# Kernel tuning notes

Hardware: AMD Instinct MI355X
Metric: run time of the kernel (lower is better)

The kernel has to match this reference:

```python
import jax, jax.numpy as jnp
from jax import lax
import numpy as np

VOCAB = 100000
EMB = 256
HID = 512          # bidirectional total
H = HID // 2       # per-direction hidden
TAGS = 12
START_IDX = 10
STOP_IDX = 11
B, S = 32, 256
NEG = -10000.0


def setup_inputs() -> dict:
    key = jax.random.key(0)
    ks = jax.random.split(key, 14)
    sc = 0.1
    sentences = jax.random.randint(ks[0], (B, S), 0, VOCAB)
    emb = jax.random.normal(ks[1], (VOCAB, EMB), jnp.float32) * sc
    wih_f = jax.random.normal(ks[2], (4 * H, EMB), jnp.float32) * sc
    whh_f = jax.random.normal(ks[3], (4 * H, H), jnp.float32) * sc
    bih_f = jax.random.normal(ks[4], (4 * H,), jnp.float32) * sc
    bhh_f = jax.random.normal(ks[5], (4 * H,), jnp.float32) * sc
    wih_b = jax.random.normal(ks[6], (4 * H, EMB), jnp.float32) * sc
    whh_b = jax.random.normal(ks[7], (4 * H, H), jnp.float32) * sc
    bih_b = jax.random.normal(ks[8], (4 * H,), jnp.float32) * sc
    bhh_b = jax.random.normal(ks[9], (4 * H,), jnp.float32) * sc
    w_out = jax.random.normal(ks[10], (TAGS, HID), jnp.float32) * sc
    b_out = jax.random.normal(ks[11], (TAGS,), jnp.float32) * sc
    transitions = jax.random.normal(ks[12], (TAGS, TAGS), jnp.float32)
    transitions = transitions.at[START_IDX, :].set(NEG)   # never transition into START
    transitions = transitions.at[:, STOP_IDX].set(NEG)    # never transition out of STOP
    return dict(sentences=sentences, emb=emb, wih_f=wih_f, whh_f=whh_f,
                bih_f=bih_f, bhh_f=bhh_f, wih_b=wih_b, whh_b=whh_b,
                bih_b=bih_b, bhh_b=bhh_b, w_out=w_out, b_out=b_out,
                transitions=transitions)


def _lstm_dir(x, wih, whh, bih, bhh, reverse):
    # x: [B,S,E]; PyTorch gate order i,f,g,o
    xg = jnp.einsum('bse,ge->bsg', x, wih) + bih + bhh  # [B,S,4H]
    h0 = jnp.zeros((x.shape[0], whh.shape[1]), x.dtype)
    c0 = jnp.zeros_like(h0)

    def step(carry, g_t):
        h, c = carry
        g = g_t + h @ whh.T
        i, f, gg, o = jnp.split(g, 4, axis=-1)
        c = jax.nn.sigmoid(f) * c + jax.nn.sigmoid(i) * jnp.tanh(gg)
        h = jax.nn.sigmoid(o) * jnp.tanh(c)
        return (h, c), h

    _, hs = lax.scan(step, (h0, c0), jnp.swapaxes(xg, 0, 1), reverse=reverse)
    return jnp.swapaxes(hs, 0, 1)  # [B,S,H]


def _features(sentences, emb, wih_f, whh_f, bih_f, bhh_f,
              wih_b, whh_b, bih_b, bhh_b, w_out, b_out):
    x = emb[sentences]                                   # [B,S,E]
    hf = _lstm_dir(x, wih_f, whh_f, bih_f, bhh_f, False)
    hb = _lstm_dir(x, wih_b, whh_b, bih_b, bhh_b, True)
    h = jnp.concatenate([hf, hb], axis=-1)               # [B,S,HID]
    return jnp.einsum('bsh,th->bst', h, w_out) + b_out   # [B,S,TAGS]


def _viterbi(feats, transitions):
    # feats: [B,S,T]; returns (score [B], path [B,S] int32)
    T = feats.shape[-1]
    init = jnp.full((T,), NEG, feats.dtype).at[START_IDX].set(0.0)

    def step(fv, emit):
        scores = fv[None, :] + transitions               # [next_tag, prev_tag]
        bp = jnp.argmax(scores, axis=1).astype(jnp.int32)
        fv_new = jnp.max(scores, axis=1) + emit
        return fv_new, bp

    def per_seq(feat_seq):                               # [S,T]
        fv, bps = lax.scan(step, init, feat_seq)         # bps: [S,T]
        term = fv + transitions[STOP_IDX]
        best = jnp.argmax(term).astype(jnp.int32)
        score = term[best]

        def back(tag, bp_t):
            return bp_t[tag], tag

        _, path = lax.scan(back, best, bps, reverse=True)
        return score, path

    return jax.vmap(per_seq)(feats)


def reference(sentences, emb, wih_f, whh_f, bih_f, bhh_f,
              wih_b, whh_b, bih_b, bhh_b, w_out, b_out, transitions):
    feats = _features(sentences, emb, wih_f, whh_f, bih_f, bhh_f,
                      wih_b, whh_b, bih_b, bhh_b, w_out, b_out)
    score, path = _viterbi(feats, transitions)
    return score, path
```

## Files before the change

### kernel.cpp

```cpp
#include <hip/hip_runtime.h>
#include <math.h>

#define BATCH 32
#define SEQ 256
#define EMBD 256
#define HDIM 256
#define G4H 1024
#define TAGS 12
#define START_IDX 10
#define STOP_IDX 11
#define NEGV -10000.0f

#define KRES 16
#define KLDS_G 18
#define KSTR_G 10

#define WS_XG    0
#define WS_X     16777216
#define WS_WPACK 18874368
#define WS_HALL  19234816
#define WS_FEATS 23429120

__device__ __forceinline__ float bcast(float v, int l) {
    return __int_as_float(__builtin_amdgcn_readlane(__float_as_int(v), l));
}

__global__ void gather_x(const int* __restrict__ sent, const float* __restrict__ emb,
                         float* __restrict__ x) {
    int m = blockIdx.x;
    int lane = threadIdx.x;
    long long row = sent[m];
    float4 v = *(const float4*)(emb + row * EMBD + lane * 4);
    *(float4*)(x + (size_t)m * EMBD + lane * 4) = v;
}

__global__ void pack_whh(const float* __restrict__ whh_f, const float* __restrict__ whh_b,
                         float4* __restrict__ pack) {
    int idx = blockIdx.x * 256 + threadIdx.x;
    if (idx >= 2 * 4 * KSTR_G * 512) return;
    int g = idx & 511;
    int r2 = idx >> 9;
    int j = r2 % KSTR_G; r2 /= KSTR_G;
    int q = r2 & 3, dir = r2 >> 2;
    int R = ((g >> 6) & 3) * 256 + q * 64 + (g & 63);
    int k = (g >> 8) * 128 + KRES + 4 * KLDS_G + 4 * j;
    const float* w = dir ? whh_b : whh_f;
    pack[idx] = *(const float4*)(w + (size_t)R * HDIM + k);
}

__launch_bounds__(256)
__global__ void gemm_xg(const float* __restrict__ x,
                        const float* __restrict__ wih_f, const float* __restrict__ wih_b,
                        const float* __restrict__ bih_f, const float* __restrict__ bhh_f,
                        const float* __restrict__ bih_b, const float* __restrict__ bhh_b,
                        float* __restrict__ xg) {
    __shared__ __align__(16) float as[8][128];
    __shared__ __align__(16) float bs[8][128];
    int m0 = blockIdx.x * 128;
    int n0 = blockIdx.y * 128;
    int tid = threadIdx.x;
    int tx = tid & 15, ty = tid >> 4;
    int lr = tid >> 1;
    int lh = (tid & 1) * 4;

    const float* arow = x + (size_t)(m0 + lr) * EMBD;
    const float* brow;
    {
        int n = n0 + lr;
        const float* w = (n < G4H) ? wih_f : wih_b;
        brow = w + (size_t)(n & 1023) * EMBD;
    }

    float acc[8][8];
    #pragma unroll
    for (int i = 0; i < 8; i++)
        #pragma unroll
        for (int j = 0; j < 8; j++) acc[i][j] = 0.f;

    for (int k0 = 0; k0 < EMBD; k0 += 8) {
        float4 av = *(const float4*)(arow + k0 + lh);
        float4 bv = *(const float4*)(brow + k0 + lh);
        __syncthreads();
        as[lh + 0][lr] = av.x; as[lh + 1][lr] = av.y; as[lh + 2][lr] = av.z; as[lh + 3][lr] = av.w;
        bs[lh + 0][lr] = bv.x; bs[lh + 1][lr] = bv.y; bs[lh + 2][lr] = bv.z; bs[lh + 3][lr] = bv.w;
        __syncthreads();
        #pragma unroll
        for (int kk = 0; kk < 8; kk++) {
            float4 a0 = *(const float4*)&as[kk][ty * 8];
            float4 a1 = *(const float4*)&as[kk][ty * 8 + 4];
            float4 b0 = *(const float4*)&bs[kk][tx * 8];
            float4 b1 = *(const float4*)&bs[kk][tx * 8 + 4];
            float a[8] = {a0.x, a0.y, a0.z, a0.w, a1.x, a1.y, a1.z, a1.w};
            float b[8] = {b0.x, b0.y, b0.z, b0.w, b1.x, b1.y, b1.z, b1.w};
            #pragma unroll
            for (int i = 0; i < 8; i++)
                #pragma unroll
                for (int j = 0; j < 8; j++) acc[i][j] += a[i] * b[j];
        }
    }

    int n = n0 + tx * 8;
    int dir = n >> 10, g0 = n & 1023;
    const float* bih = dir ? bih_b : bih_f;
    const float* bhh = dir ? bhh_b : bhh_f;
    float bi[8], bh[8];
    #pragma unroll
    for (int j = 0; j < 8; j++) { bi[j] = bih[g0 + j]; bh[j] = bhh[g0 + j]; }
    float* ob = xg + (size_t)dir * 8192 * G4H;
    #pragma unroll
    for (int i = 0; i < 8; i++) {
        int m = m0 + ty * 8 + i;
        float v[8];
        #pragma unroll
        for (int j = 0; j < 8; j++) v[j] = (acc[i][j] + bi[j]) + bh[j];
        *(float4*)(ob + (size_t)m * G4H + g0)     = make_float4(v[0], v[1], v[2], v[3]);
        *(float4*)(ob + (size_t)m * G4H + g0 + 4) = make_float4(v[4], v[5], v[6], v[7]);
    }
}

__global__ void zero_sync(float* __restrict__ hx, int* __restrict__ flags) {
    int i = blockIdx.x * 256 + threadIdx.x;
    if (i < 64 * 512) hx[i] = 0.f;
    if (i < 64 * 4) flags[i] = 0;
}

#define DOT4(W, KL)                                              \
    a0 += (W).x * bcast(hv[((KL) + 0) >> 6], ((KL) + 0) & 63);   \
    a1 += (W).y * bcast(hv[((KL) + 1) >> 6], ((KL) + 1) & 63);   \
    a2 += (W).z * bcast(hv[((KL) + 2) >> 6], ((KL) + 2) & 63);   \
    a3 += (W).w * bcast(hv[((KL) + 3) >> 6], ((KL) + 3) & 63);

__launch_bounds__(512)
__global__ void lstm_rec(const float* __restrict__ xg,
                         const float* __restrict__ whh_f, const float* __restrict__ whh_b,
                         const float4* __restrict__ wpack,
                         float* __restrict__ h_all,
                         float* __restrict__ hx, int* __restrict__ flags) {
    int blk = blockIdx.x;
    int chain = blk & 63;
    int q = blk >> 6;
    int dir = chain & 1, b = chain >> 1;
    int g = threadIdx.x;
    int lane = g & 63;
    int r = g & 255;
    int kh = g >> 8;
    int G = r >> 6, ul = r & 63;
    int R = G * 256 + q * 64 + ul;

    const float* whh = dir ? whh_b : whh_f;
    const float* wrow = whh + (size_t)R * HDIM + kh * 128;
    const float4* wp = wpack + (size_t)(dir * 4 + q) * KSTR_G * 512 + g;
    const float* xgb = xg + (size_t)dir * 8192 * G4H + (size_t)b * SEQ * G4H + R;
    float* hxc = hx + chain * 512;
    int* fl = flags + chain * 4;

    __shared__ __align__(16) float4 wlds[KLDS_G * 512];
    __shared__ float part[512];

    #pragma unroll
    for (int j = 0; j < KLDS_G; j++)
        wlds[j * 512 + g] = *(const float4*)(wrow + KRES + j * 4);
    float4 wr[KRES / 4];
    #pragma unroll
    for (int i = 0; i < KRES / 4; i++)
        wr[i] = *(const float4*)(wrow + i * 4);

    float c = 0.f;
    __syncthreads();

    for (int t = 0; t < SEQ; t++) {
        int s = dir ? (SEQ - 1 - t) : t;

        float xval = 0.f;
        if (g < 256) xval = xgb[(size_t)s * G4H];
        float4 sb[4];
        #pragma unroll
        for (int p = 0; p < 4; p++) sb[p] = wp[(size_t)p * 512];

        if (t > 0) {
            if (g < 3) {
                int pq = g + (g >= q ? 1 : 0);
                while (__hip_atomic_load(fl + pq, __ATOMIC_ACQUIRE,
                                         __HIP_MEMORY_SCOPE_AGENT) < t) {}
            }
            __syncthreads();
        }

        int rp = (t + 1) & 1;
        float hv[2];
        #pragma unroll
        for (int j = 0; j < 2; j++)
            hv[j] = __hip_atomic_load(hxc + rp * 256 + kh * 128 + j * 64 + lane,
                                      __ATOMIC_RELAXED, __HIP_MEMORY_SCOPE_AGENT);

        float a0 = 0.f, a1 = 0.f, a2 = 0.f, a3 = 0.f;

        #pragma unroll
        for (int i = 0; i < KRES / 4; i++) {
            float4 w = wr[i];
            DOT4(w, i * 4)
        }
        #pragma unroll
        for (int j = 0; j < KLDS_G; j++) {
            float4 w = wlds[j * 512 + g];
            DOT4(w, KRES + j * 4)
        }
        #pragma unroll
        for (int j = 0; j < KSTR_G; j++) {
            float4 w = sb[j & 3];
            if (j + 4 < KSTR_G) sb[j & 3] = wp[(size_t)(j + 4) * 512];
            DOT4(w, KRES + 4 * KLDS_G + j * 4)
        }

        part[g] = (a0 + a1) + (a2 + a3);
        __syncthreads();
        if (g < 256) part[g] = part[g] + part[g + 256] + xval;
        __syncthreads();
        if (g < 64) {
            float gi = part[g], gf = part[64 + g], gg = part[128 + g], go = part[192 + g];
            float si = 1.f / (1.f + expf(-gi));
            float sf = 1.f / (1.f + expf(-gf));
            float so = 1.f / (1.f + expf(-go));
            c = sf * c + si * tanhf(gg);
            float h = so * tanhf(c);
            int u = q * 64 + g;
            h_all[((size_t)b * SEQ + s) * 512 + dir * HDIM + u] = h;
            __hip_atomic_store(hxc + (t & 1) * 256 + u, h,
                               __ATOMIC_RELAXED, __HIP_MEMORY_SCOPE_AGENT);
        }
        __syncthreads();
        if (g == 0)
            __hip_atomic_store(fl + q, t + 1,
                               __ATOMIC_RELEASE, __HIP_MEMORY_SCOPE_AGENT);
    }
}

__global__ void feats_kernel(const float* __restrict__ h_all, const float* __restrict__ w_out,
                             const float* __restrict__ b_out, float* __restrict__ feats) {
    int p = blockIdx.x;
    int lane = threadIdx.x;
    const float* h = h_all + (size_t)p * 512;
    for (int f = 0; f < TAGS; f++) {
        float s = 0.f;
        const float* w = w_out + f * 512;
        #pragma unroll
        for (int k = 0; k < 512; k += 64) s += h[k + lane] * w[k + lane];
        #pragma unroll
        for (int off = 32; off; off >>= 1) s += __shfl_down(s, off);
        if (lane == 0) feats[(size_t)p * TAGS + f] = s + b_out[f];
    }
}

__global__ void viterbi_kernel(const float* __restrict__ feats, const float* __restrict__ trans,
                               float* __restrict__ out) {
    int b = blockIdx.x;
    int t = threadIdx.x;
    __shared__ float fv[TAGS], fvn[TAGS], tr[TAGS * TAGS];
    __shared__ int bp[SEQ][TAGS];

    for (int i = t; i < TAGS * TAGS; i += 64) tr[i] = trans[i];
    if (t < TAGS) fv[t] = (t == START_IDX) ? 0.f : NEGV;
    __syncthreads();

    const float* fb = feats + (size_t)b * SEQ * TAGS;
    for (int s = 0; s < SEQ; s++) {
        if (t < TAGS) {
            float best = fv[0] + tr[t * TAGS + 0];
            int bi = 0;
            #pragma unroll
            for (int prev = 1; prev < TAGS; prev++) {
                float v = fv[prev] + tr[t * TAGS + prev];
                if (v > best) { best = v; bi = prev; }
            }
            bp[s][t] = bi;
            fvn[t] = best + fb[s * TAGS + t];
        }
        __syncthreads();
        if (t < TAGS) fv[t] = fvn[t];
        __syncthreads();
    }

    if (t == 0) {
        float best = fv[0] + tr[STOP_IDX * TAGS + 0];
        int bi = 0;
        #pragma unroll
        for (int p = 1; p < TAGS; p++) {
            float v = fv[p] + tr[STOP_IDX * TAGS + p];
            if (v > best) { best = v; bi = p; }
        }
        out[b] = best;
        float* path = out + BATCH + (size_t)b * SEQ;
        int tag = bi;
        path[SEQ - 1] = (float)tag;
        for (int s = SEQ - 1; s >= 1; s--) {
            tag = bp[s][tag];
            path[s - 1] = (float)tag;
        }
    }
}

extern "C" void kernel_launch(void* const* d_in, const int* in_sizes, int n_in,
                              void* d_out, int out_size, void* d_ws, size_t ws_size,
                              hipStream_t stream) {
    const int*   sent  = (const int*)d_in[0];
    const float* emb   = (const float*)d_in[1];
    const float* wih_f = (const float*)d_in[2];
    const float* whh_f = (const float*)d_in[3];
    const float* bih_f = (const float*)d_in[4];
    const float* bhh_f = (const float*)d_in[5];
    const float* wih_b = (const float*)d_in[6];
    const float* whh_b = (const float*)d_in[7];
    const float* bih_b = (const float*)d_in[8];
    const float* bhh_b = (const float*)d_in[9];
    const float* w_out = (const float*)d_in[10];
    const float* b_out = (const float*)d_in[11];
    const float* trans = (const float*)d_in[12];
    float* ws    = (float*)d_ws;
    float* xg    = ws + WS_XG;
    float* x     = ws + WS_X;
    float* wpack = ws + WS_WPACK;
    float* h_all = ws + WS_HALL;
    float* feats = ws + WS_FEATS;
    float* hx    = ws + WS_X;
    int*   flags = (int*)(ws + WS_X + 64 * 512);
    float* out   = (float*)d_out;

    gather_x<<<BATCH * SEQ, 64, 0, stream>>>(sent, emb, x);
    pack_whh<<<(2 * 4 * KSTR_G * 512 + 255) / 256, 256, 0, stream>>>(whh_f, whh_b, (float4*)wpack);
    gemm_xg<<<dim3(64, 16), 256, 0, stream>>>(x, wih_f, wih_b, bih_f, bhh_f, bih_b, bhh_b, xg);
    zero_sync<<<128, 256, 0, stream>>>(hx, flags);
    lstm_rec<<<256, 512, 0, stream>>>(xg, whh_f, whh_b, (const float4*)wpack, h_all, hx, flags);
    feats_kernel<<<BATCH * SEQ, 64, 0, stream>>>(h_all, w_out, b_out, feats);
    viterbi_kernel<<<BATCH, 64, 0, stream>>>(feats, trans, out);
}
```

Measured before the change: 1.776 ms.

## Keep all recurrent weights on-chip, drop streamed weight pack and trim syncs

Raises the register-resident slice of the recurrent weight matrix from 16 to 56 columns per thread. Together with the 72 columns already in LDS, each thread's 128-column slice now lives entirely on-chip, so the per-step streaming of packed weights from global memory and the pack_whh kernel are removed. It also removes one barrier by adding xval before the partial reduction, switches the spin-wait to relaxed loads followed by a single acquire fence, and moves the h_all store after the flag release. The cost is much higher register pressure at 512 threads per block, which could cause spills.

```diff
diff --git a/kernel.cpp b/kernel.cpp
--- a/kernel.cpp
+++ b/kernel.cpp
@@ -11,13 +11,11 @@
 #define STOP_IDX 11
 #define NEGV -10000.0f
 
-#define KRES 16
+#define KRES 56
 #define KLDS_G 18
-#define KSTR_G 10
 
 #define WS_XG    0
 #define WS_X     16777216
-#define WS_WPACK 18874368
 #define WS_HALL  19234816
 #define WS_FEATS 23429120
 
@@ -32,20 +30,6 @@
     long long row = sent[m];
     float4 v = *(const float4*)(emb + row * EMBD + lane * 4);
     *(float4*)(x + (size_t)m * EMBD + lane * 4) = v;
-}
-
-__global__ void pack_whh(const float* __restrict__ whh_f, const float* __restrict__ whh_b,
-                         float4* __restrict__ pack) {
-    int idx = blockIdx.x * 256 + threadIdx.x;
-    if (idx >= 2 * 4 * KSTR_G * 512) return;
-    int g = idx & 511;
-    int r2 = idx >> 9;
-    int j = r2 % KSTR_G; r2 /= KSTR_G;
-    int q = r2 & 3, dir = r2 >> 2;
-    int R = ((g >> 6) & 3) * 256 + q * 64 + (g & 63);
-    int k = (g >> 8) * 128 + KRES + 4 * KLDS_G + 4 * j;
-    const float* w = dir ? whh_b : whh_f;
-    pack[idx] = *(const float4*)(w + (size_t)R * HDIM + k);
 }
 
 __launch_bounds__(256)
@@ -133,7 +117,6 @@
 __launch_bounds__(512)
 __global__ void lstm_rec(const float* __restrict__ xg,
                          const float* __restrict__ whh_f, const float* __restrict__ whh_b,
-                         const float4* __restrict__ wpack,
                          float* __restrict__ h_all,
                          float* __restrict__ hx, int* __restrict__ flags) {
     int blk = blockIdx.x;
@@ -149,7 +132,6 @@
 
     const float* whh = dir ? whh_b : whh_f;
     const float* wrow = whh + (size_t)R * HDIM + kh * 128;
-    const float4* wp = wpack + (size_t)(dir * 4 + q) * KSTR_G * 512 + g;
     const float* xgb = xg + (size_t)dir * 8192 * G4H + (size_t)b * SEQ * G4H + R;
     float* hxc = hx + chain * 512;
     int* fl = flags + chain * 4;
@@ -173,17 +155,15 @@
 
         float xval = 0.f;
         if (g < 256) xval = xgb[(size_t)s * G4H];
-        float4 sb[4];
-        #pragma unroll
-        for (int p = 0; p < 4; p++) sb[p] = wp[(size_t)p * 512];
 
         if (t > 0) {
             if (g < 3) {
                 int pq = g + (g >= q ? 1 : 0);
-                while (__hip_atomic_load(fl + pq, __ATOMIC_ACQUIRE,
+                while (__hip_atomic_load(fl + pq, __ATOMIC_RELAXED,
                                          __HIP_MEMORY_SCOPE_AGENT) < t) {}
             }
             __syncthreads();
+            __builtin_amdgcn_fence(__ATOMIC_ACQUIRE, "agent");
         }
 
         int rp = (t + 1) & 1;
@@ -205,33 +185,29 @@
             float4 w = wlds[j * 512 + g];
             DOT4(w, KRES + j * 4)
         }
-        #pragma unroll
-        for (int j = 0; j < KSTR_G; j++) {
-            float4 w = sb[j & 3];
-            if (j + 4 < KSTR_G) sb[j & 3] = wp[(size_t)(j + 4) * 512];
-            DOT4(w, KRES + 4 * KLDS_G + j * 4)
-        }
-
-        part[g] = (a0 + a1) + (a2 + a3);
-        __syncthreads();
-        if (g < 256) part[g] = part[g] + part[g + 256] + xval;
-        __syncthreads();
+
+        part[g] = (a0 + a1) + (a2 + a3) + xval;
+        __syncthreads();
+        float h = 0.f;
         if (g < 64) {
-            float gi = part[g], gf = part[64 + g], gg = part[128 + g], go = part[192 + g];
+            float gi = part[g]       + part[g + 256];
+            float gf = part[g + 64]  + part[g + 320];
+            float gg = part[g + 128] + part[g + 384];
+            float go = part[g + 192] + part[g + 448];
             float si = 1.f / (1.f + expf(-gi));
             float sf = 1.f / (1.f + expf(-gf));
             float so = 1.f / (1.f + expf(-go));
             c = sf * c + si * tanhf(gg);
-            float h = so * tanhf(c);
-            int u = q * 64 + g;
-            h_all[((size_t)b * SEQ + s) * 512 + dir * HDIM + u] = h;
-            __hip_atomic_store(hxc + (t & 1) * 256 + u, h,
+            h = so * tanhf(c);
+            __hip_atomic_store(hxc + (t & 1) * 256 + q * 64 + g, h,
                                __ATOMIC_RELAXED, __HIP_MEMORY_SCOPE_AGENT);
         }
         __syncthreads();
         if (g == 0)
             __hip_atomic_store(fl + q, t + 1,
                                __ATOMIC_RELEASE, __HIP_MEMORY_SCOPE_AGENT);
+        if (g < 64)
+            h_all[((size_t)b * SEQ + s) * 512 + dir * HDIM + q * 64 + g] = h;
     }
 }
 
@@ -318,7 +294,6 @@
     float* ws    = (float*)d_ws;
     float* xg    = ws + WS_XG;
     float* x     = ws + WS_X;
-    float* wpack = ws + WS_WPACK;
     float* h_all = ws + WS_HALL;
     float* feats = ws + WS_FEATS;
     float* hx    = ws + WS_X;
@@ -326,10 +301,9 @@
     float* out   = (float*)d_out;
 
     gather_x<<<BATCH * SEQ, 64, 0, stream>>>(sent, emb, x);
-    pack_whh<<<(2 * 4 * KSTR_G * 512 + 255) / 256, 256, 0, stream>>>(whh_f, whh_b, (float4*)wpack);
     gemm_xg<<<dim3(64, 16), 256, 0, stream>>>(x, wih_f, wih_b, bih_f, bhh_f, bih_b, bhh_b, xg);
     zero_sync<<<128, 256, 0, stream>>>(hx, flags);
-    lstm_rec<<<256, 512, 0, stream>>>(xg, whh_f, whh_b, (const float4*)wpack, h_all, hx, flags);
+    lstm_rec<<<256, 512, 0, stream>>>(xg, whh_f, whh_b, h_all, hx, flags);
     feats_kernel<<<BATCH * SEQ, 64, 0, stream>>>(h_all, w_out, b_out, feats);
     viterbi_kernel<<<BATCH, 64, 0, stream>>>(feats, trans, out);
 }
```

After: 4.729 ms. 2.66x slower.
